# Optimization experiments

Hardware: AMD Instinct MI355X
Metric: run time of the kernel (lower is better)

The kernel has to match this reference:

```python
import jax, jax.numpy as jnp
import numpy as np

KERNEL_MUL = 2.0
KERNEL_NUM = 5


def _mmd_channel(s, t):
    """Multi-bandwidth Gaussian-kernel MMD for one channel. s,t: [B, D]."""
    B = s.shape[0]
    total = jnp.concatenate([s, t], axis=0)            # [2B, D]
    sq = jnp.sum(total * total, axis=1)                # [2B]
    # ||xi - xj||^2 via Gram identity (avoids [2B,2B,D] intermediate)
    L2 = sq[:, None] + sq[None, :] - 2.0 * (total @ total.T)  # [2B, 2B]
    n = 2 * B
    # torch uses L2_distance.data -> bandwidth is detached
    bandwidth = jax.lax.stop_gradient(jnp.sum(L2)) / (n * n - n)
    bandwidth = bandwidth / (KERNEL_MUL ** (KERNEL_NUM // 2))
    bws = bandwidth * (KERNEL_MUL ** jnp.arange(KERNEL_NUM, dtype=s.dtype))  # [K_num]
    kernels = jnp.sum(jnp.exp(-L2[None, :, :] / bws[:, None, None]), axis=0)  # [2B, 2B]
    XX = kernels[:B, :B]
    YY = kernels[B:, B:]
    XY = kernels[:B, B:]
    YX = kernels[B:, :B]
    return jnp.mean(XX + YY - XY - YX)


def setup_inputs() -> dict:
    key = jax.random.key(0)
    k1, k2 = jax.random.split(key)
    B, K, H, W = 128, 21, 64, 64
    source = jax.random.normal(k1, (B, K, H, W), dtype=jnp.float32)
    target = jax.random.normal(k2, (B, K, H, W), dtype=jnp.float32)
    return {"source": source, "target": target}


def reference(source, target):
    B, K = source.shape[0], source.shape[1]
    s = source.reshape(B, K, -1)  # [B, K, D]
    t = target.reshape(B, K, -1)
    per_channel = jax.vmap(_mmd_channel, in_axes=(1, 1))(s, t)  # [K]
    return jnp.sum(per_channel) / K
```

## Files before the change

kernel.cpp:

```cpp
#include <hip/hip_runtime.h>
#include <hip/hip_bf16.h>
#include <stdint.h>

typedef __attribute__((ext_vector_type(4))) float f32x4;
typedef __attribute__((ext_vector_type(8))) short bf16x8;

#define NCH 21
#define NROW 256
#define DIM 4096
#define BK 64
#define NTILE 10

__device__ const int g_TI[NTILE] = {0, 0, 0, 0, 1, 1, 1, 2, 2, 3};
__device__ const int g_TJ[NTILE] = {0, 1, 2, 3, 1, 2, 3, 2, 3, 3};

typedef const __attribute__((address_space(1))) uint32_t gas_u32;
typedef __attribute__((address_space(3))) uint32_t las_u32;

__device__ __forceinline__ uint32_t pack_bf2(float x, float y) {
  __hip_bfloat162 h = __float22bfloat162_rn(float2{x, y});
  union { __hip_bfloat162 h; uint32_t u; } c;
  c.h = h;
  return c.u;
}

__device__ __forceinline__ int lds_foff(int row, int fcol) {
  return row * 64 + ((((fcol >> 2) ^ (row & 7)) & 15) << 2);
}

__global__ __launch_bounds__(512, 4) void gram_kernel(
    const float* __restrict__ src, const float* __restrict__ tgt,
    float* __restrict__ Gp, int kshift, int kchunk) {
  const int P = 1 << kshift;
  const int NG = NCH << kshift;
  const int q = NG >> 3, r8 = NG & 7;
  const int x = blockIdx.x & 7;
  const int slot = blockIdx.x >> 3;
  const int cnt = q + (x < r8 ? 1 : 0);
  if (slot >= cnt * 3) return;
  const int gbase = (x < r8) ? x * (q + 1) : r8 * (q + 1) + (x - r8) * q;
  const int gi = slot / 3;
  const int bt = slot - gi * 3;
  const int g = gbase + gi;
  const int ch = g >> kshift;
  const int ks = g & (P - 1);
  const int kbase = ks * kchunk;
  const int row_base = (bt == 1) ? 128 : 0;
  const int col_base = (bt == 0) ? 0 : 128;
  const bool isdiag = (bt != 2);
  const int tid = threadIdx.x;
  const int lane = tid & 63;
  const int wave = tid >> 6;

  __shared__ __attribute__((aligned(16))) float AsF[128 * 64];
  __shared__ __attribute__((aligned(16))) float BsF[128 * 64];

  f32x4 acc[2][4];
#pragma unroll
  for (int m = 0; m < 2; ++m)
#pragma unroll
    for (int n = 0; n < 4; ++n)
      acc[m][n] = (f32x4){0.f, 0.f, 0.f, 0.f};

  const int wr = (wave >> 1) * 32;
  const int wc = (wave & 1) * 64;

  const float* Ab = row_base ? tgt : src;
  const float* Bb = col_base ? tgt : src;
  const float* gA[4];
  const float* gB[4];
#pragma unroll
  for (int i = 0; i < 4; ++i) {
    const int id = i * 512 + tid;
    const int row = id >> 4;
    const int csw = ((id & 15) ^ (row & 7)) * 4;
    gA[i] = Ab + ((size_t)row * NCH + ch) * DIM + kbase + csw;
    gB[i] = Bb + ((size_t)row * NCH + ch) * DIM + kbase + csw;
  }

  const int nk = kchunk / BK;

  for (int it = 0; it < nk; ++it) {
    const int ko = it * BK;
#pragma unroll
    for (int i = 0; i < 4; ++i) {
      __builtin_amdgcn_global_load_lds(
          (gas_u32*)(const void*)(gA[i] + ko),
          (las_u32*)(void*)(AsF + i * 2048 + wave * 256), 16, 0, 0);
    }
    if (!isdiag) {
#pragma unroll
      for (int i = 0; i < 4; ++i) {
        __builtin_amdgcn_global_load_lds(
            (gas_u32*)(const void*)(gB[i] + ko),
            (las_u32*)(void*)(BsF + i * 2048 + wave * 256), 16, 0, 0);
      }
    }
    __syncthreads();

    const float* Bsrc = isdiag ? AsF : BsF;
#pragma unroll
    for (int kk = 0; kk < 2; ++kk) {
      const int kf = kk * 32 + (lane >> 4) * 8;
      bf16x8 a[2], b[4];
#pragma unroll
      for (int m = 0; m < 2; ++m) {
        const int row = wr + m * 16 + (lane & 15);
        f32x4 x0 = *reinterpret_cast<const f32x4*>(&AsF[lds_foff(row, kf)]);
        f32x4 x1 = *reinterpret_cast<const f32x4*>(&AsF[lds_foff(row, kf + 4)]);
        union { bf16x8 v; uint32_t u[4]; } cv;
        cv.u[0] = pack_bf2(x0.x, x0.y);
        cv.u[1] = pack_bf2(x0.z, x0.w);
        cv.u[2] = pack_bf2(x1.x, x1.y);
        cv.u[3] = pack_bf2(x1.z, x1.w);
        a[m] = cv.v;
      }
#pragma unroll
      for (int n = 0; n < 4; ++n) {
        const int row = wc + n * 16 + (lane & 15);
        f32x4 x0 = *reinterpret_cast<const f32x4*>(&Bsrc[lds_foff(row, kf)]);
        f32x4 x1 = *reinterpret_cast<const f32x4*>(&Bsrc[lds_foff(row, kf + 4)]);
        union { bf16x8 v; uint32_t u[4]; } cv;
        cv.u[0] = pack_bf2(x0.x, x0.y);
        cv.u[1] = pack_bf2(x0.z, x0.w);
        cv.u[2] = pack_bf2(x1.x, x1.y);
        cv.u[3] = pack_bf2(x1.z, x1.w);
        b[n] = cv.v;
      }
#pragma unroll
      for (int m = 0; m < 2; ++m)
#pragma unroll
        for (int n = 0; n < 4; ++n)
          acc[m][n] = __builtin_amdgcn_mfma_f32_16x16x32_bf16(a[m], b[n],
                                                              acc[m][n], 0, 0, 0);
    }
    __syncthreads();
  }

  float* gp = Gp + (size_t)(ch * P + ks) * (NROW * NROW);
#pragma unroll
  for (int m = 0; m < 2; ++m)
#pragma unroll
    for (int n = 0; n < 4; ++n) {
      const int grow = row_base + wr + m * 16 + ((lane >> 4) << 2);
      const int gcol = col_base + wc + n * 16 + (lane & 15);
      if ((grow >> 6) > (gcol >> 6)) continue;
#pragma unroll
      for (int j = 0; j < 4; ++j)
        gp[(size_t)(grow + j) * NROW + gcol] = acc[m][n][j];
    }
}

__device__ __forceinline__ float block_sum256(float v, float* sm) {
#pragma unroll
  for (int o = 32; o > 0; o >>= 1) v += __shfl_down(v, o, 64);
  const int lane = threadIdx.x & 63;
  const int wv = threadIdx.x >> 6;
  if (lane == 0) sm[wv] = v;
  __syncthreads();
  float r = 0.f;
  if (threadIdx.x == 0) r = sm[0] + sm[1] + sm[2] + sm[3];
  __syncthreads();
  return r;
}

__global__ __launch_bounds__(256) void foldsum_kernel(
    const f32x4* __restrict__ Gp, f32x4* __restrict__ Gf,
    float* __restrict__ sums, int P) {
  const int t = blockIdx.x;
  const int ch = blockIdx.y;
  const int ti = g_TI[t], tj = g_TJ[t];
  const bool isdiag = (ti == tj);
  const int tid = threadIdx.x;
  float s = 0.f, tr = 0.f;
#pragma unroll
  for (int i = 0; i < 4; ++i) {
    const int idx4 = tid * 4 + i;
    const int rrow = idx4 >> 4;
    const int c4 = idx4 & 15;
    const int base_v = (ti * 64 + rrow) * 64 + tj * 16 + c4;
    f32x4 v = Gp[(size_t)(ch * P) * 16384 + base_v];
    for (int p = 1; p < P; ++p) v += Gp[(size_t)(ch * P + p) * 16384 + base_v];
    Gf[(size_t)ch * 16384 + base_v] = v;
    s += (v.x + v.y) + (v.z + v.w);
    if (isdiag) {
      const int cb = c4 * 4;
#pragma unroll
      for (int e = 0; e < 4; ++e)
        if (cb + e == rrow) tr += v[e];
    }
  }
  __shared__ float sm[4];
  float sG = block_sum256(s, sm);
  float sT = block_sum256(tr, sm);
  if (tid == 0) {
    sums[ch * 20 + t] = sG;
    if (isdiag) sums[ch * 20 + 10 + ti] = sT;
  }
}

__global__ __launch_bounds__(256) void mmd_kernel(const float* __restrict__ Gf,
                                                  const float* __restrict__ sums,
                                                  float* __restrict__ partial) {
  const int t = blockIdx.x;
  const int ch = blockIdx.y;
  const int ti = g_TI[t], tj = g_TJ[t];
  const int tid = threadIdx.x;
  const float* gg = Gf + (size_t)ch * (NROW * NROW);

  const float* sc = sums + ch * 20;
  float sumG = 0.f;
#pragma unroll
  for (int k = 0; k < NTILE; ++k)
    sumG += (g_TI[k] == g_TJ[k] ? 1.f : 2.f) * sc[k];
  const float trace = (sc[10] + sc[11]) + (sc[12] + sc[13]);
  const float sumL2 = 2.f * NROW * trace - 2.f * sumG;
  const float bw = sumL2 / (float)(NROW * NROW - NROW) * 0.25f;
  float inv[5];
#pragma unroll
  for (int a = 0; a < 5; ++a) inv[a] = -1.f / (bw * (float)(1 << a));

  __shared__ float dA[64], dB[64];
  if (tid < 64) dA[tid] = gg[(size_t)(ti * 64 + tid) * (NROW + 1)];
  else if (tid < 128) dB[tid - 64] = gg[(size_t)(tj * 64 + (tid - 64)) * (NROW + 1)];
  __syncthreads();

  const int col = tid & 63;
  const int qq = tid >> 6;
  const float dj = dB[col];
  float acc = 0.f;
#pragma unroll 4
  for (int it = 0; it < 16; ++it) {
    const int r = it * 4 + qq;
    const float L2 = dA[r] + dj - 2.f * gg[(size_t)(ti * 64 + r) * NROW + tj * 64 + col];
    float kv = 0.f;
#pragma unroll
    for (int a = 0; a < 5; ++a) kv += __expf(L2 * inv[a]);
    acc += kv;
  }
  __shared__ float sm[4];
  float tot = block_sum256(acc, sm);
  if (tid == 0) {
    float wgt = (ti == tj) ? 1.f : 2.f;
    float sgn = ((ti >= 2) == (tj >= 2)) ? 1.f : -1.f;
    partial[ch * NTILE + t] = tot * wgt * sgn;
  }
}

__global__ __launch_bounds__(256) void final_kernel(const float* __restrict__ partial,
                                                    float* __restrict__ out) {
  const int tid = threadIdx.x;
  float v = (tid < NCH * NTILE) ? partial[tid] : 0.f;
  __shared__ float sm[4];
  float tot = block_sum256(v, sm);
  if (tid == 0) out[0] = tot * (1.f / (NCH * 128.f * 128.f));
}

extern "C" void kernel_launch(void* const* d_in, const int* in_sizes, int n_in,
                              void* d_out, int out_size, void* d_ws, size_t ws_size,
                              hipStream_t stream) {
  const float* src = (const float*)d_in[0];
  const float* tgt = (const float*)d_in[1];
  float* out = (float*)d_out;
  const size_t GSZ = (size_t)NROW * NROW;

  int kshift = 0;
  if (ws_size >= (NCH * 9 * GSZ + 512) * sizeof(float)) kshift = 3;
  else if (ws_size >= (NCH * 5 * GSZ + 512) * sizeof(float)) kshift = 2;
  else if (ws_size >= (NCH * 3 * GSZ + 512) * sizeof(float)) kshift = 1;
  const int P = 1 << kshift;

  float* Gp = (float*)d_ws;
  float* Gf = (P > 1) ? Gp + (size_t)NCH * P * GSZ : Gp;
  float* sums = Gf + (size_t)NCH * GSZ;
  float* partial = sums + NCH * 20;

  const int NG = NCH * P;
  const int q = NG / 8, r8 = NG % 8;
  const int grid = 8 * (q + (r8 ? 1 : 0)) * 3;

  gram_kernel<<<dim3(grid), 512, 0, stream>>>(src, tgt, Gp, kshift, DIM >> kshift);
  foldsum_kernel<<<dim3(NTILE, NCH), 256, 0, stream>>>((const f32x4*)Gp,
                                                       (f32x4*)Gf, sums, P);
  mmd_kernel<<<dim3(NTILE, NCH), 256, 0, stream>>>(Gf, sums, partial);
  final_kernel<<<1, 256, 0, stream>>>(partial, out);
}
```

Measured before the change: 48.33 us.

## Compute full 256-row Gram per block with bf16 LDS staging and register prefetch

```diff
diff --git a/kernel.cpp b/kernel.cpp
--- a/kernel.cpp
+++ b/kernel.cpp
@@ -14,9 +14,6 @@
 __device__ const int g_TI[NTILE] = {0, 0, 0, 0, 1, 1, 1, 2, 2, 3};
 __device__ const int g_TJ[NTILE] = {0, 1, 2, 3, 1, 2, 3, 2, 3, 3};
 
-typedef const __attribute__((address_space(1))) uint32_t gas_u32;
-typedef __attribute__((address_space(3))) uint32_t las_u32;
-
 __device__ __forceinline__ uint32_t pack_bf2(float x, float y) {
   __hip_bfloat162 h = __float22bfloat162_rn(float2{x, y});
   union { __hip_bfloat162 h; uint32_t u; } c;
@@ -24,131 +21,109 @@
   return c.u;
 }
 
-__device__ __forceinline__ int lds_foff(int row, int fcol) {
-  return row * 64 + ((((fcol >> 2) ^ (row & 7)) & 15) << 2);
-}
-
-__global__ __launch_bounds__(512, 4) void gram_kernel(
+__global__ __launch_bounds__(1024, 4) void gram_kernel(
     const float* __restrict__ src, const float* __restrict__ tgt,
     float* __restrict__ Gp, int kshift, int kchunk) {
   const int P = 1 << kshift;
-  const int NG = NCH << kshift;
-  const int q = NG >> 3, r8 = NG & 7;
-  const int x = blockIdx.x & 7;
-  const int slot = blockIdx.x >> 3;
-  const int cnt = q + (x < r8 ? 1 : 0);
-  if (slot >= cnt * 3) return;
-  const int gbase = (x < r8) ? x * (q + 1) : r8 * (q + 1) + (x - r8) * q;
-  const int gi = slot / 3;
-  const int bt = slot - gi * 3;
-  const int g = gbase + gi;
+  const int g = blockIdx.x;
   const int ch = g >> kshift;
   const int ks = g & (P - 1);
   const int kbase = ks * kchunk;
-  const int row_base = (bt == 1) ? 128 : 0;
-  const int col_base = (bt == 0) ? 0 : 128;
-  const bool isdiag = (bt != 2);
   const int tid = threadIdx.x;
   const int lane = tid & 63;
   const int wave = tid >> 6;
 
-  __shared__ __attribute__((aligned(16))) float AsF[128 * 64];
-  __shared__ __attribute__((aligned(16))) float BsF[128 * 64];
-
-  f32x4 acc[2][4];
-#pragma unroll
-  for (int m = 0; m < 2; ++m)
+  __shared__ __attribute__((aligned(16))) ushort S[256 * 64];
+
+  f32x4 acc[4][4];
+#pragma unroll
+  for (int m = 0; m < 4; ++m)
 #pragma unroll
     for (int n = 0; n < 4; ++n)
       acc[m][n] = (f32x4){0.f, 0.f, 0.f, 0.f};
 
-  const int wr = (wave >> 1) * 32;
-  const int wc = (wave & 1) * 64;
-
-  const float* Ab = row_base ? tgt : src;
-  const float* Bb = col_base ? tgt : src;
-  const float* gA[4];
-  const float* gB[4];
+  const float* gptr[4];
+  int lw[4];
 #pragma unroll
   for (int i = 0; i < 4; ++i) {
-    const int id = i * 512 + tid;
+    const int id = i * 1024 + tid;
     const int row = id >> 4;
-    const int csw = ((id & 15) ^ (row & 7)) * 4;
-    gA[i] = Ab + ((size_t)row * NCH + ch) * DIM + kbase + csw;
-    gB[i] = Bb + ((size_t)row * NCH + ch) * DIM + kbase + csw;
-  }
+    const int c16 = id & 15;
+    const float* base = (row < 128) ? src + ((size_t)row * NCH + ch) * DIM
+                                    : tgt + ((size_t)(row - 128) * NCH + ch) * DIM;
+    gptr[i] = base + kbase + c16 * 4;
+    const int sch = (c16 >> 1) ^ (row & 7);
+    lw[i] = row * 64 + sch * 8 + (c16 & 1) * 4;
+  }
+
+  const int ti = g_TI[wave < NTILE ? wave : 0];
+  const int tj = g_TJ[wave < NTILE ? wave : 0];
 
   const int nk = kchunk / BK;
 
+  f32x4 v[4];
+#pragma unroll
+  for (int i = 0; i < 4; ++i) v[i] = *reinterpret_cast<const f32x4*>(gptr[i]);
+
   for (int it = 0; it < nk; ++it) {
-    const int ko = it * BK;
+    __syncthreads();
 #pragma unroll
     for (int i = 0; i < 4; ++i) {
-      __builtin_amdgcn_global_load_lds(
-          (gas_u32*)(const void*)(gA[i] + ko),
-          (las_u32*)(void*)(AsF + i * 2048 + wave * 256), 16, 0, 0);
-    }
-    if (!isdiag) {
-#pragma unroll
-      for (int i = 0; i < 4; ++i) {
-        __builtin_amdgcn_global_load_lds(
-            (gas_u32*)(const void*)(gB[i] + ko),
-            (las_u32*)(void*)(BsF + i * 2048 + wave * 256), 16, 0, 0);
+      uint2 wv;
+      wv.x = pack_bf2(v[i].x, v[i].y);
+      wv.y = pack_bf2(v[i].z, v[i].w);
+      *reinterpret_cast<uint2*>(&S[lw[i]]) = wv;
+    }
+    if (it + 1 < nk) {
+      const int ko = (it + 1) * BK;
+#pragma unroll
+      for (int i = 0; i < 4; ++i)
+        v[i] = *reinterpret_cast<const f32x4*>(gptr[i] + ko);
+    }
+    asm volatile("s_waitcnt lgkmcnt(0)" ::: "memory");
+    __builtin_amdgcn_s_barrier();
+    asm volatile("" ::: "memory");
+
+    if (wave < NTILE) {
+#pragma unroll
+      for (int kk = 0; kk < 2; ++kk) {
+        const int chunk = kk * 4 + (lane >> 4);
+        bf16x8 a[4], b[4];
+#pragma unroll
+        for (int m = 0; m < 4; ++m) {
+          const int row = ti * 64 + m * 16 + (lane & 15);
+          a[m] = *reinterpret_cast<const bf16x8*>(
+              &S[row * 64 + (chunk ^ (row & 7)) * 8]);
+        }
+#pragma unroll
+        for (int n = 0; n < 4; ++n) {
+          const int row = tj * 64 + n * 16 + (lane & 15);
+          b[n] = *reinterpret_cast<const bf16x8*>(
+              &S[row * 64 + (chunk ^ (row & 7)) * 8]);
+        }
+#pragma unroll
+        for (int m = 0; m < 4; ++m)
+#pragma unroll
+          for (int n = 0; n < 4; ++n)
+            acc[m][n] = __builtin_amdgcn_mfma_f32_16x16x32_bf16(a[m], b[n],
+                                                                acc[m][n], 0, 0, 0);
       }
     }
-    __syncthreads();
-
-    const float* Bsrc = isdiag ? AsF : BsF;
-#pragma unroll
-    for (int kk = 0; kk < 2; ++kk) {
-      const int kf = kk * 32 + (lane >> 4) * 8;
-      bf16x8 a[2], b[4];
-#pragma unroll
-      for (int m = 0; m < 2; ++m) {
-        const int row = wr + m * 16 + (lane & 15);
-        f32x4 x0 = *reinterpret_cast<const f32x4*>(&AsF[lds_foff(row, kf)]);
-        f32x4 x1 = *reinterpret_cast<const f32x4*>(&AsF[lds_foff(row, kf + 4)]);
-        union { bf16x8 v; uint32_t u[4]; } cv;
-        cv.u[0] = pack_bf2(x0.x, x0.y);
-        cv.u[1] = pack_bf2(x0.z, x0.w);
-        cv.u[2] = pack_bf2(x1.x, x1.y);
-        cv.u[3] = pack_bf2(x1.z, x1.w);
-        a[m] = cv.v;
+  }
+
+  if (wave < NTILE) {
+    float* gp = Gp + (size_t)(ch * P + ks) * (NROW * NROW);
+#pragma unroll
+    for (int m = 0; m < 4; ++m)
+#pragma unroll
+      for (int n = 0; n < 4; ++n) {
+        const int grow = ti * 64 + m * 16 + ((lane >> 4) << 2);
+        const int gcol = tj * 64 + n * 16 + (lane & 15);
+#pragma unroll
+        for (int j = 0; j < 4; ++j)
+          gp[(size_t)(grow + j) * NROW + gcol] = acc[m][n][j];
       }
-#pragma unroll
-      for (int n = 0; n < 4; ++n) {
-        const int row = wc + n * 16 + (lane & 15);
-        f32x4 x0 = *reinterpret_cast<const f32x4*>(&Bsrc[lds_foff(row, kf)]);
-        f32x4 x1 = *reinterpret_cast<const f32x4*>(&Bsrc[lds_foff(row, kf + 4)]);
-        union { bf16x8 v; uint32_t u[4]; } cv;
-        cv.u[0] = pack_bf2(x0.x, x0.y);
-        cv.u[1] = pack_bf2(x0.z, x0.w);
-        cv.u[2] = pack_bf2(x1.x, x1.y);
-        cv.u[3] = pack_bf2(x1.z, x1.w);
-        b[n] = cv.v;
-      }
-#pragma unroll
-      for (int m = 0; m < 2; ++m)
-#pragma unroll
-        for (int n = 0; n < 4; ++n)
-          acc[m][n] = __builtin_amdgcn_mfma_f32_16x16x32_bf16(a[m], b[n],
-                                                              acc[m][n], 0, 0, 0);
-    }
-    __syncthreads();
-  }
-
-  float* gp = Gp + (size_t)(ch * P + ks) * (NROW * NROW);
-#pragma unroll
-  for (int m = 0; m < 2; ++m)
-#pragma unroll
-    for (int n = 0; n < 4; ++n) {
-      const int grow = row_base + wr + m * 16 + ((lane >> 4) << 2);
-      const int gcol = col_base + wc + n * 16 + (lane & 15);
-      if ((grow >> 6) > (gcol >> 6)) continue;
-#pragma unroll
-      for (int j = 0; j < 4; ++j)
-        gp[(size_t)(grow + j) * NROW + gcol] = acc[m][n][j];
-    }
+  }
 }
 
 __device__ __forceinline__ float block_sum256(float v, float* sm) {
@@ -275,11 +250,8 @@
   float* sums = Gf + (size_t)NCH * GSZ;
   float* partial = sums + NCH * 20;
 
-  const int NG = NCH * P;
-  const int q = NG / 8, r8 = NG % 8;
-  const int grid = 8 * (q + (r8 ? 1 : 0)) * 3;
-
-  gram_kernel<<<dim3(grid), 512, 0, stream>>>(src, tgt, Gp, kshift, DIM >> kshift);
+  gram_kernel<<<dim3(NCH * P), 1024, 0, stream>>>(src, tgt, Gp, kshift,
+                                                  DIM >> kshift);
   foldsum_kernel<<<dim3(NTILE, NCH), 256, 0, stream>>>((const f32x4*)Gp,
                                                        (f32x4*)Gf, sums, P);
   mmd_kernel<<<dim3(NTILE, NCH), 256, 0, stream>>>(Gf, sums, partial);
```

After: 44.15 us. 8.6% less time.
